# Performance work log

Measured on AMD Instinct MI355X. Metric: run time of the kernel, lower is better.

Reference implementation:

```python
import jax, jax.numpy as jnp
import numpy as np

N = 50000
E = 800000

def _glorot(k, shape):
    lim = float(np.sqrt(6.0 / (shape[0] + shape[1])))
    return jax.random.uniform(k, shape, jnp.float32, -lim, lim)

def setup_inputs() -> dict:
    key = jax.random.key(0)
    ks = jax.random.split(key, 12)
    x = jax.random.normal(ks[0], (N, 58), jnp.float32)
    edge_index = jax.random.randint(ks[1], (2, E), 0, N, jnp.int32)
    neg_edge_index = jax.random.randint(ks[2], (2, E), 0, N, jnp.int32)
    return dict(
        x=x, edge_index=edge_index, neg_edge_index=neg_edge_index,
        W1_0=_glorot(ks[3], (58, 300)), W1_1=_glorot(ks[4], (58, 300)), b1=jnp.zeros((300,), jnp.float32),
        W2_0=_glorot(ks[5], (300, 100)), W2_1=_glorot(ks[6], (300, 100)), b2=jnp.zeros((100,), jnp.float32),
        W3_0=_glorot(ks[7], (100, 1)), W3_1=_glorot(ks[8], (100, 1)), b3=jnp.zeros((1,), jnp.float32),
        lin1_W=_glorot(ks[9], (100, 58)), lin1_b=jnp.zeros((100,), jnp.float32),
        lin2_W=_glorot(ks[10], (100, 58)), lin2_b=jnp.zeros((100,), jnp.float32),
        c1=jnp.full((1,), 0.5, jnp.float32), c2=jnp.full((1,), 0.5, jnp.float32),
    )

def _cheb(x, src, dst, norm, W0, W1, b):
    tx1 = jax.ops.segment_sum(x[src] * norm[:, None], dst, num_segments=x.shape[0])
    return x @ W0 + tx1 @ W1 + b

def reference(x, edge_index, neg_edge_index,
              W1_0, W1_1, b1, W2_0, W2_1, b2, W3_0, W3_1, b3,
              lin1_W, lin1_b, lin2_W, lin2_b, c1, c2):
    src, dst = edge_index[0], edge_index[1]
    deg = jax.ops.segment_sum(jnp.ones((E,), x.dtype), src, num_segments=N)
    dis = jnp.where(deg > 0, 1.0 / jnp.sqrt(jnp.where(deg > 0, deg, 1.0)), 0.0)
    norm = -(dis[src] * dis[dst])  # [E]
    h = jax.nn.relu(_cheb(x, src, dst, norm, W1_0, W1_1, b1))      # [N,300]
    x1 = jax.nn.relu(_cheb(h, src, dst, norm, W2_0, W2_1, b2))     # [N,100]
    xm = x1 + jax.nn.relu(x @ lin1_W.T + lin1_b)
    z = x1 + jax.nn.relu(x @ lin2_W.T + lin2_b)
    pos_score = jnp.sum(z[edge_index[0]] * z[edge_index[1]], axis=1)
    pos_loss = -jnp.mean(jnp.log(jax.nn.sigmoid(pos_score) + 1e-15))
    neg_score = jnp.sum(z[neg_edge_index[0]] * z[neg_edge_index[1]], axis=1)
    neg_loss = -jnp.mean(jnp.log(1.0 - jax.nn.sigmoid(neg_score) + 1e-15))
    r_loss = pos_loss + neg_loss
    out = _cheb(xm, src, dst, norm, W3_0, W3_1, b3)                # [N,1]
    return (out, r_loss, c1, c2)
```

## Files before the change

### kernel.cpp

```cpp
#include <hip/hip_runtime.h>
#include <math.h>

#define NN 50000
#define NE 800000
#define SB 1024
#define CAP 64

using bf16x8 = __attribute__((ext_vector_type(8))) short;
using f32x4  = __attribute__((ext_vector_type(4))) float;
using f32x2  = __attribute__((ext_vector_type(2))) float;
using i32x8  = __attribute__((ext_vector_type(8))) int;

__device__ __forceinline__ float b2f(short s) {
    union { unsigned u; float f; } v;
    v.u = ((unsigned)(unsigned short)s) << 16;
    return v.f;
}
__device__ __forceinline__ unsigned short f2b(float f) {
    union { float f; unsigned u; } v;
    v.f = f;
    unsigned r = v.u + 0x7fffu + ((v.u >> 16) & 1u);
    return (unsigned short)(r >> 16);
}
__device__ __forceinline__ unsigned char f2e4m3(float f) {
    return (unsigned char)(__builtin_amdgcn_cvt_pk_fp8_f32(f, f, 0, false) & 0xff);
}

__global__ void k_degs(const int* __restrict__ ei, int* __restrict__ degs) {
    int e = blockIdx.x * 256 + threadIdx.x;
    if (e < NE) atomicAdd(&degs[ei[e]], 1);
}

__global__ __launch_bounds__(256) void k_prep(const float* __restrict__ x,
                                              unsigned short* __restrict__ xcat,
                                              unsigned char* __restrict__ xf8,
                                              const int* __restrict__ degs,
                                              float* __restrict__ dis,
                                              const float* __restrict__ W1_0,
                                              const float* __restrict__ W1_1,
                                              const float* __restrict__ W2_0,
                                              const float* __restrict__ W2_1,
                                              const float* __restrict__ L1,
                                              const float* __restrict__ L2,
                                              unsigned short* __restrict__ Wt1f,
                                              unsigned short* __restrict__ Wt2f,
                                              unsigned short* __restrict__ Wtlf) {
    int b = blockIdx.x;
    if (b < 12500) {
        int t = b * 256 + threadIdx.x;
        int n = t >> 6, k = t & 63;
        float v = (k < 58) ? x[(size_t)n * 58 + k] : 0.0f;
        xcat[(size_t)n * 128 + k] = f2b(v);
        xf8[(size_t)n * 64 + k] = f2e4m3(v);
        return;
    }
    if (b < 12696) {
        int i = (b - 12500) * 256 + threadIdx.x;
        if (i < NN) {
            float d = (float)degs[i];
            dis[i] = d > 0.0f ? 1.0f / sqrtf(d) : 0.0f;
        }
        return;
    }
    int t = (b - 12696) * 256 + threadIdx.x;
    if (t < 40960) {
        int f = t >> 9, lane = (t >> 3) & 63, j = t & 7;
        int nt = f >> 2, s = f & 3;
        int ml = lane & 15, quad = lane >> 4;
        int k = s * 32 + quad * 8 + j;
        int col = nt * 16 + ml;
        float v = 0.0f;
        if (col < 300) {
            if (k < 58) v = W1_0[k * 300 + col];
            else if (k >= 64 && k < 122) v = W1_1[(k - 64) * 300 + col];
        }
        Wt1f[t] = f2b(v);
    } else if (t < 107520) {
        int u = t - 40960;
        int f = u >> 9, lane = (u >> 3) & 63, j = u & 7;
        int nt = f / 10, s = f - nt * 10;
        int ml = lane & 15, quad = lane >> 4;
        int k = s * 32 + quad * 8 + j;
        int col = nt * 16 + ml;
        float v = 0.0f;
        if (k < 300) {
            if (col < 100) v = W2_0[k * 100 + col];
            else if (col >= 104 && col < 204) v = W2_1[k * 100 + (col - 104)];
        }
        Wt2f[u] = f2b(v);
    } else if (t < 120832) {
        int u = t - 107520;
        int f = u >> 9, lane = (u >> 3) & 63, j = u & 7;
        int nt = f >> 1, s = f & 1;
        int ml = lane & 15, quad = lane >> 4;
        int k = s * 32 + quad * 8 + j;
        int col = nt * 16 + ml;
        float v = 0.0f;
        if (k < 58) {
            if (col < 100) v = L1[col * 58 + k];
            else if (col >= 104 && col < 204) v = L2[(col - 104) * 58 + k];
        }
        Wtlf[u] = f2b(v);
    }
}

__global__ void k_fillbkt(const int* __restrict__ ei, const float* __restrict__ dis,
                          int* __restrict__ cnt, unsigned* __restrict__ bkt) {
    int e = blockIdx.x * 256 + threadIdx.x;
    if (e < NE) {
        int s = ei[e], d = ei[NE + e];
        int slot = atomicAdd(&cnt[d], 1);
        if (slot < CAP) {
            float nm = -(dis[s] * dis[d]);
            bkt[(d << 6) + slot] = ((unsigned)f2b(nm) << 16) | (unsigned)s;
        }
    }
}

__global__ __launch_bounds__(256) void k_gather58(const int* __restrict__ cnt,
                                                  const unsigned* __restrict__ bkt,
                                                  const unsigned char* __restrict__ xf8,
                                                  unsigned short* __restrict__ xcat) {
    int t = blockIdx.x * 256 + threadIdx.x;
    int n = t >> 3, l = t & 7;
    if (n >= NN) return;
    int c = cnt[n]; if (c > CAP) c = CAP;
    int base = n << 6;
    float acc[8] = {0, 0, 0, 0, 0, 0, 0, 0};
    for (int i = 0; i < c; i++) {
        unsigned pv = bkt[base + i];
        float cc = b2f((short)(pv >> 16));
        uint2 u = *(const uint2*)(xf8 + (size_t)(pv & 0xFFFFu) * 64 + l * 8);
        f32x2 p0 = __builtin_amdgcn_cvt_pk_f32_fp8(u.x, false);
        f32x2 p1 = __builtin_amdgcn_cvt_pk_f32_fp8(u.x, true);
        f32x2 p2 = __builtin_amdgcn_cvt_pk_f32_fp8(u.y, false);
        f32x2 p3 = __builtin_amdgcn_cvt_pk_f32_fp8(u.y, true);
        acc[0] += cc * p0.x; acc[1] += cc * p0.y;
        acc[2] += cc * p1.x; acc[3] += cc * p1.y;
        acc[4] += cc * p2.x; acc[5] += cc * p2.y;
        acc[6] += cc * p3.x; acc[7] += cc * p3.y;
    }
    bf16x8 o;
#pragma unroll
    for (int j = 0; j < 8; j++) o[j] = (short)f2b(acc[j]);
    *(bf16x8*)(xcat + (size_t)n * 128 + 64 + l * 8) = o;
}

__global__ __launch_bounds__(256) void k_mm12(const unsigned short* __restrict__ xcat,
                                              const unsigned short* __restrict__ Wt1f,
                                              const float* __restrict__ b1,
                                              const unsigned short* __restrict__ Wt2f,
                                              float* __restrict__ hp,
                                              unsigned char* __restrict__ hwf8) {
    __shared__ __attribute__((aligned(16))) unsigned short hs[64 * 328];
    __shared__ __attribute__((aligned(16))) unsigned short bst[2][5120];
    int tid = threadIdx.x;
    int wave = tid >> 6, lane = tid & 63, ml = lane & 15, quad = lane >> 4;
    int row0 = blockIdx.x * 64;
    int rw = row0 + wave * 16;

    int ar = rw + ml; if (ar >= NN) ar = NN - 1;
    const bf16x8* Ap = (const bf16x8*)(xcat + (size_t)ar * 128 + quad * 8);
    bf16x8 a0 = Ap[0], a1 = Ap[4], a2 = Ap[8], a3 = Ap[12];

    ((bf16x8*)bst[0])[tid] = ((const bf16x8*)Wt1f)[tid];
    __syncthreads();

    for (int nt = 0; nt < 20; nt++) {
        if (nt + 1 < 20)
            ((bf16x8*)bst[(nt + 1) & 1])[tid] =
                ((const bf16x8*)(Wt1f + (size_t)(nt + 1) * 2048))[tid];
        const bf16x8* Bp = (const bf16x8*)bst[nt & 1];
        f32x4 acc = {0.f, 0.f, 0.f, 0.f};
        acc = __builtin_amdgcn_mfma_f32_16x16x32_bf16(a0, Bp[0 * 64 + lane], acc, 0, 0, 0);
        acc = __builtin_amdgcn_mfma_f32_16x16x32_bf16(a1, Bp[1 * 64 + lane], acc, 0, 0, 0);
        acc = __builtin_amdgcn_mfma_f32_16x16x32_bf16(a2, Bp[2 * 64 + lane], acc, 0, 0, 0);
        acc = __builtin_amdgcn_mfma_f32_16x16x32_bf16(a3, Bp[3 * 64 + lane], acc, 0, 0, 0);
        int col = nt * 16 + ml;
        float bias = (col < 300) ? b1[col] : 0.0f;
#pragma unroll
        for (int r = 0; r < 4; r++) {
            float v = acc[r] + bias;
            v = v > 0.0f ? v : 0.0f;
            if (col >= 300) v = 0.0f;
            hs[(wave * 16 + quad * 4 + r) * 328 + col] = f2b(v);
        }
        __syncthreads();
    }

    for (int i = tid; i < 640; i += 256)
        ((bf16x8*)bst[0])[i] = ((const bf16x8*)Wt2f)[i];
    bf16x8 A2[10];
#pragma unroll
    for (int s = 0; s < 10; s++)
        A2[s] = *(const bf16x8*)(hs + (wave * 16 + ml) * 328 + s * 32 + quad * 8);
    __syncthreads();

    for (int nt = 0; nt < 13; nt++) {
        if (nt + 1 < 13)
            for (int i = tid; i < 640; i += 256)
                ((bf16x8*)bst[(nt + 1) & 1])[i] =
                    ((const bf16x8*)(Wt2f + (size_t)(nt + 1) * 5120))[i];
        const bf16x8* Bp = (const bf16x8*)bst[nt & 1];
        f32x4 acc = {0.f, 0.f, 0.f, 0.f};
#pragma unroll
        for (int s = 0; s < 10; s++)
            acc = __builtin_amdgcn_mfma_f32_16x16x32_bf16(A2[s], Bp[s * 64 + lane], acc, 0, 0, 0);
        int j = nt * 16 + ml;
#pragma unroll
        for (int r = 0; r < 4; r++) {
            int row = rw + quad * 4 + r;
            if (row < NN) {
                if (j < 104) hp[(size_t)row * 104 + j] = acc[r];
                else hwf8[(size_t)row * 128 + (j - 104)] = f2e4m3(acc[r]);
            }
        }
        __syncthreads();
    }
}

__global__ __launch_bounds__(256) void k_gather100(const int* __restrict__ cnt,
                                                   const unsigned* __restrict__ bkt,
                                                   const unsigned char* __restrict__ hwf8,
                                                   float* __restrict__ tx2) {
    int t = blockIdx.x * 256 + threadIdx.x;
    int n = t >> 4, l = t & 15;
    if (n >= NN || l >= 13) return;
    int c = cnt[n]; if (c > CAP) c = CAP;
    int base = n << 6;
    float acc[8] = {0, 0, 0, 0, 0, 0, 0, 0};
    for (int i = 0; i < c; i++) {
        unsigned pv = bkt[base + i];
        float cc = b2f((short)(pv >> 16));
        uint2 u = *(const uint2*)(hwf8 + (size_t)(pv & 0xFFFFu) * 128 + l * 8);
        f32x2 p0 = __builtin_amdgcn_cvt_pk_f32_fp8(u.x, false);
        f32x2 p1 = __builtin_amdgcn_cvt_pk_f32_fp8(u.x, true);
        f32x2 p2 = __builtin_amdgcn_cvt_pk_f32_fp8(u.y, false);
        f32x2 p3 = __builtin_amdgcn_cvt_pk_f32_fp8(u.y, true);
        acc[0] += cc * p0.x; acc[1] += cc * p0.y;
        acc[2] += cc * p1.x; acc[3] += cc * p1.y;
        acc[4] += cc * p2.x; acc[5] += cc * p2.y;
        acc[6] += cc * p3.x; acc[7] += cc * p3.y;
    }
    f32x4 o0 = {acc[0], acc[1], acc[2], acc[3]};
    f32x4 o1 = {acc[4], acc[5], acc[6], acc[7]};
    *(f32x4*)(tx2 + (size_t)n * 104 + l * 8) = o0;
    *(f32x4*)(tx2 + (size_t)n * 104 + l * 8 + 4) = o1;
}

__global__ __launch_bounds__(256) void k_mmlin(const unsigned short* __restrict__ xcat,
                                               const unsigned short* __restrict__ Wtlf,
                                               const float* __restrict__ hp,
                                               const float* __restrict__ tx2,
                                               const float* __restrict__ b2,
                                               const float* __restrict__ l1b,
                                               const float* __restrict__ l2b,
                                               float* __restrict__ xm,
                                               unsigned char* __restrict__ zf8) {
    int wave = threadIdx.x >> 6, lane = threadIdx.x & 63;
    int row0 = blockIdx.x * 64 + wave * 16;
    if (row0 >= NN) return;
    int ml = lane & 15, quad = lane >> 4;
    const bf16x8* Ap = (const bf16x8*)(xcat + (size_t)(row0 + ml) * 128 + quad * 8);
    bf16x8 a0 = Ap[0], a1 = Ap[4];
    for (int nt = 0; nt < 13; nt++) {
        bf16x8 b0 = *(const bf16x8*)(Wtlf + (size_t)((nt * 2 + 0) * 64 + lane) * 8);
        bf16x8 b1f = *(const bf16x8*)(Wtlf + (size_t)((nt * 2 + 1) * 64 + lane) * 8);
        f32x4 acc = {0.f, 0.f, 0.f, 0.f};
        acc = __builtin_amdgcn_mfma_f32_16x16x32_bf16(a0, b0, acc, 0, 0, 0);
        acc = __builtin_amdgcn_mfma_f32_16x16x32_bf16(a1, b1f, acc, 0, 0, 0);
        int j = nt * 16 + ml;
        int jj = (j < 104) ? j : j - 104;
        float bb = 0.0f, lb = 0.0f;
        if (jj < 100) {
            bb = b2[jj];
            lb = (j < 104) ? l1b[jj] : l2b[jj];
        }
#pragma unroll
        for (int r = 0; r < 4; r++) {
            int row = row0 + quad * 4 + r;
            float x1v = hp[(size_t)row * 104 + jj] + tx2[(size_t)row * 104 + jj] + bb;
            x1v = x1v > 0.0f ? x1v : 0.0f;
            float lv = acc[r] + lb;
            lv = lv > 0.0f ? lv : 0.0f;
            float o = x1v + lv;
            if (j < 104) xm[(size_t)row * 104 + j] = o;
            else zf8[(size_t)row * 128 + (j - 104)] = f2e4m3(o);
        }
    }
}

__global__ __launch_bounds__(256) void k_score_l3(const unsigned char* __restrict__ zf8,
                                                  const int* __restrict__ ei,
                                                  const int* __restrict__ nei,
                                                  double* __restrict__ red,
                                                  const float* __restrict__ xm,
                                                  const float* __restrict__ W30,
                                                  const float* __restrict__ W31,
                                                  const float* __restrict__ b3,
                                                  float* __restrict__ out,
                                                  float* __restrict__ s) {
    int tid = threadIdx.x;
    int lane = tid & 63;
    int wid = (blockIdx.x * 256 + tid) >> 6;
    int nw = SB * 4;
    int ml = lane & 15, quad = lane >> 4;
    int dr = ml - quad * 4;
    bool diag = (dr >= 0 && dr < 4);
    float facc = 0.0f;
    const int G = (2 * NE) / 16;
    for (int g = wid; g < G; g += nw) {
        int base = g * 16;
        int a, b;
        if (base < NE) {
            a = ei[base + ml];
            b = ei[NE + base + ml];
        } else {
            a = nei[base - NE + ml];
            b = nei[base + ml];
        }
        i32x8 av = *(const i32x8*)(zf8 + (size_t)a * 128 + quad * 32);
        i32x8 bv = *(const i32x8*)(zf8 + (size_t)b * 128 + quad * 32);
        f32x4 d = {0.f, 0.f, 0.f, 0.f};
        d = __builtin_amdgcn_mfma_scale_f32_16x16x128_f8f6f4(
                av, bv, d, 0, 0, 0, 0x7f7f7f7f, 0, 0x7f7f7f7f);
        if (diag) {
            float p = d[dr];
            float sg = 1.0f / (1.0f + expf(-p));
            float term = (base < NE) ? logf(sg + 1e-15f) : logf(1.0f - sg + 1e-15f);
            facc += term;
        }
    }
    int l32 = tid & 31;
    int gslot = (blockIdx.x * 256 + tid) >> 5;
    for (int n = gslot; n < NN; n += SB * 8) {
        const float* row = xm + (size_t)n * 104;
        float d0 = 0.0f, d1 = 0.0f;
        for (int k = l32; k < 100; k += 32) {
            float v = row[k];
            d0 += v * W30[k];
            d1 += v * W31[k];
        }
        for (int off = 16; off; off >>= 1) {
            d0 += __shfl_down(d0, off, 32);
            d1 += __shfl_down(d1, off, 32);
        }
        if (l32 == 0) {
            out[n] = d0 + b3[0];
            s[n] = d1;
        }
    }
    __shared__ double sred[256];
    sred[tid] = (double)facc;
    __syncthreads();
    for (int st = 128; st; st >>= 1) {
        if (tid < st) sred[tid] += sred[tid + st];
        __syncthreads();
    }
    if (tid == 0) red[blockIdx.x] = sred[0];
}

__global__ __launch_bounds__(256) void k_final_g1(const double* __restrict__ red,
                                                  const float* __restrict__ c1,
                                                  const float* __restrict__ c2,
                                                  const int* __restrict__ cnt,
                                                  const unsigned* __restrict__ bkt,
                                                  const float* __restrict__ s,
                                                  float* __restrict__ out) {
    if (blockIdx.x == 0) {
        double a = 0.0;
        for (int i = threadIdx.x; i < SB; i += 256) a += red[i];
        __shared__ double sred[256];
        sred[threadIdx.x] = a;
        __syncthreads();
        for (int st = 128; st; st >>= 1) {
            if (threadIdx.x < st) sred[threadIdx.x] += sred[threadIdx.x + st];
            __syncthreads();
        }
        if (threadIdx.x == 0) {
            out[NN] = (float)(-sred[0] / (double)NE);
            out[NN + 1] = c1[0];
            out[NN + 2] = c2[0];
        }
        return;
    }
    int n = (blockIdx.x - 1) * 256 + threadIdx.x;
    if (n >= NN) return;
    int c = cnt[n]; if (c > CAP) c = CAP;
    int base = n << 6;
    float acc = 0.0f;
    for (int i = 0; i < c; i++) {
        unsigned pv = bkt[base + i];
        acc += b2f((short)(pv >> 16)) * s[pv & 0xFFFFu];
    }
    out[n] += acc;
}

extern "C" void kernel_launch(void* const* d_in, const int* in_sizes, int n_in,
                              void* d_out, int out_size, void* d_ws, size_t ws_size,
                              hipStream_t stream) {
    const float* x    = (const float*)d_in[0];
    const int*   ei   = (const int*)d_in[1];
    const int*   nei  = (const int*)d_in[2];
    const float* W1_0 = (const float*)d_in[3];
    const float* W1_1 = (const float*)d_in[4];
    const float* b1   = (const float*)d_in[5];
    const float* W2_0 = (const float*)d_in[6];
    const float* W2_1 = (const float*)d_in[7];
    const float* b2   = (const float*)d_in[8];
    const float* W3_0 = (const float*)d_in[9];
    const float* W3_1 = (const float*)d_in[10];
    const float* b3   = (const float*)d_in[11];
    const float* l1W  = (const float*)d_in[12];
    const float* l1b  = (const float*)d_in[13];
    const float* l2W  = (const float*)d_in[14];
    const float* l2b  = (const float*)d_in[15];
    const float* c1   = (const float*)d_in[16];
    const float* c2   = (const float*)d_in[17];
    float* out = (float*)d_out;
    float* w = (float*)d_ws;

    unsigned*       bkt    = (unsigned*)w;
    int*            degs   = (int*)(w + 3200000);
    int*            cnt    = (int*)(w + 3250000);
    float*          dis    = w + 3300000;
    float*          sbuf   = w + 3350000;
    double*         red    = (double*)(w + 3400000);
    unsigned short* xcat   = (unsigned short*)(w + 3402048);
    unsigned short* Wt1f   = (unsigned short*)(w + 6602048);
    unsigned short* Wt2f   = (unsigned short*)(w + 6622528);
    unsigned short* Wtlf   = (unsigned short*)(w + 6655808);
    float*          hp     = w + 6662464;
    unsigned char*  hwf8   = (unsigned char*)(w + 11862464);
    float*          xm     = w + 13462464;
    unsigned char*  zf8    = (unsigned char*)(w + 18662464);
    unsigned char*  xf8    = (unsigned char*)(w + 20262464);
    float*          tx2    = w + 21062464;

    hipMemsetAsync(degs, 0, 100000 * sizeof(int), stream);

    k_degs<<<(NE + 255) / 256, 256, 0, stream>>>(ei, degs);
    k_prep<<<13168, 256, 0, stream>>>(x, xcat, xf8, degs, dis,
                                      W1_0, W1_1, W2_0, W2_1, l1W, l2W,
                                      Wt1f, Wt2f, Wtlf);
    k_fillbkt<<<(NE + 255) / 256, 256, 0, stream>>>(ei, dis, cnt, bkt);

    k_gather58<<<(NN * 8 + 255) / 256, 256, 0, stream>>>(cnt, bkt, xf8, xcat);
    k_mm12<<<(NN + 63) / 64, 256, 0, stream>>>(xcat, Wt1f, b1, Wt2f, hp, hwf8);

    k_gather100<<<NN * 16 / 256, 256, 0, stream>>>(cnt, bkt, hwf8, tx2);
    k_mmlin<<<(NN + 63) / 64, 256, 0, stream>>>(xcat, Wtlf, hp, tx2, b2, l1b, l2b, xm, zf8);

    k_score_l3<<<SB, 256, 0, stream>>>(zf8, ei, nei, red, xm, W3_0, W3_1, b3, out, sbuf);
    k_final_g1<<<1 + (NN + 255) / 256, 256, 0, stream>>>(red, c1, c2, cnt, bkt, sbuf, out);
}
```

Baseline: 382.1 us.

## Factor edge norm into node scaling, fuse gather100 into mmlin, split score/loss

The symmetric normalization is factored into per-node scaling: source features are pre-scaled by dis[src] and the aggregate is scaled by -dis[dst]. Buckets therefore store only 16-bit source indices, and degree counting and bucket fill merge into one kernel. The layer-2 gather moves into the linear/epilogue kernel through shared memory, and the W3 projection is done there too, so the tx2 and xm round trips disappear. Edge scoring now writes raw scores to a buffer and a separate loss kernel reduces them. This adds an extra pass over 1.6M floats and extra launches, and fp8 quantization now applies to scaled values.

```diff
diff --git a/kernel.cpp b/kernel.cpp
--- a/kernel.cpp
+++ b/kernel.cpp
@@ -3,7 +3,8 @@
 
 #define NN 50000
 #define NE 800000
-#define SB 1024
+#define SB2 2048
+#define LB 1024
 #define CAP 64
 
 using bf16x8 = __attribute__((ext_vector_type(8))) short;
@@ -25,10 +26,26 @@
 __device__ __forceinline__ unsigned char f2e4m3(float f) {
     return (unsigned char)(__builtin_amdgcn_cvt_pk_fp8_f32(f, f, 0, false) & 0xff);
 }
-
-__global__ void k_degs(const int* __restrict__ ei, int* __restrict__ degs) {
+__device__ __forceinline__ void acc8(float* acc, uint2 u) {
+    f32x2 p0 = __builtin_amdgcn_cvt_pk_f32_fp8(u.x, false);
+    f32x2 p1 = __builtin_amdgcn_cvt_pk_f32_fp8(u.x, true);
+    f32x2 p2 = __builtin_amdgcn_cvt_pk_f32_fp8(u.y, false);
+    f32x2 p3 = __builtin_amdgcn_cvt_pk_f32_fp8(u.y, true);
+    acc[0] += p0.x; acc[1] += p0.y;
+    acc[2] += p1.x; acc[3] += p1.y;
+    acc[4] += p2.x; acc[5] += p2.y;
+    acc[6] += p3.x; acc[7] += p3.y;
+}
+
+__global__ void k_build(const int* __restrict__ ei, int* __restrict__ degs,
+                        int* __restrict__ cnt, unsigned short* __restrict__ bkt16) {
     int e = blockIdx.x * 256 + threadIdx.x;
-    if (e < NE) atomicAdd(&degs[ei[e]], 1);
+    if (e < NE) {
+        int s = ei[e], d = ei[NE + e];
+        atomicAdd(&degs[s], 1);
+        int slot = atomicAdd(&cnt[d], 1);
+        if (slot < CAP) bkt16[(d << 6) + slot] = (unsigned short)s;
+    }
 }
 
 __global__ __launch_bounds__(256) void k_prep(const float* __restrict__ x,
@@ -51,14 +68,16 @@
         int n = t >> 6, k = t & 63;
         float v = (k < 58) ? x[(size_t)n * 58 + k] : 0.0f;
         xcat[(size_t)n * 128 + k] = f2b(v);
-        xf8[(size_t)n * 64 + k] = f2e4m3(v);
+        int dg = degs[n];
+        float dv = dg > 0 ? 1.0f / sqrtf((float)dg) : 0.0f;
+        xf8[(size_t)n * 64 + k] = f2e4m3(dv * v);
         return;
     }
     if (b < 12696) {
         int i = (b - 12500) * 256 + threadIdx.x;
         if (i < NN) {
-            float d = (float)degs[i];
-            dis[i] = d > 0.0f ? 1.0f / sqrtf(d) : 0.0f;
+            int dg = degs[i];
+            dis[i] = dg > 0 ? 1.0f / sqrtf((float)dg) : 0.0f;
         }
         return;
     }
@@ -104,45 +123,26 @@
     }
 }
 
-__global__ void k_fillbkt(const int* __restrict__ ei, const float* __restrict__ dis,
-                          int* __restrict__ cnt, unsigned* __restrict__ bkt) {
-    int e = blockIdx.x * 256 + threadIdx.x;
-    if (e < NE) {
-        int s = ei[e], d = ei[NE + e];
-        int slot = atomicAdd(&cnt[d], 1);
-        if (slot < CAP) {
-            float nm = -(dis[s] * dis[d]);
-            bkt[(d << 6) + slot] = ((unsigned)f2b(nm) << 16) | (unsigned)s;
-        }
-    }
-}
-
 __global__ __launch_bounds__(256) void k_gather58(const int* __restrict__ cnt,
-                                                  const unsigned* __restrict__ bkt,
+                                                  const unsigned short* __restrict__ bkt16,
+                                                  const float* __restrict__ dis,
                                                   const unsigned char* __restrict__ xf8,
                                                   unsigned short* __restrict__ xcat) {
     int t = blockIdx.x * 256 + threadIdx.x;
     int n = t >> 3, l = t & 7;
     if (n >= NN) return;
     int c = cnt[n]; if (c > CAP) c = CAP;
-    int base = n << 6;
+    float dn = dis[n];
+    const unsigned short* bp = bkt16 + (n << 6);
     float acc[8] = {0, 0, 0, 0, 0, 0, 0, 0};
     for (int i = 0; i < c; i++) {
-        unsigned pv = bkt[base + i];
-        float cc = b2f((short)(pv >> 16));
-        uint2 u = *(const uint2*)(xf8 + (size_t)(pv & 0xFFFFu) * 64 + l * 8);
-        f32x2 p0 = __builtin_amdgcn_cvt_pk_f32_fp8(u.x, false);
-        f32x2 p1 = __builtin_amdgcn_cvt_pk_f32_fp8(u.x, true);
-        f32x2 p2 = __builtin_amdgcn_cvt_pk_f32_fp8(u.y, false);
-        f32x2 p3 = __builtin_amdgcn_cvt_pk_f32_fp8(u.y, true);
-        acc[0] += cc * p0.x; acc[1] += cc * p0.y;
-        acc[2] += cc * p1.x; acc[3] += cc * p1.y;
-        acc[4] += cc * p2.x; acc[5] += cc * p2.y;
-        acc[6] += cc * p3.x; acc[7] += cc * p3.y;
+        unsigned src = bp[i];
+        uint2 u = *(const uint2*)(xf8 + (size_t)src * 64 + l * 8);
+        acc8(acc, u);
     }
     bf16x8 o;
 #pragma unroll
-    for (int j = 0; j < 8; j++) o[j] = (short)f2b(acc[j]);
+    for (int j = 0; j < 8; j++) o[j] = (short)f2b(-dn * acc[j]);
     *(bf16x8*)(xcat + (size_t)n * 128 + 64 + l * 8) = o;
 }
 
@@ -150,6 +150,7 @@
                                               const unsigned short* __restrict__ Wt1f,
                                               const float* __restrict__ b1,
                                               const unsigned short* __restrict__ Wt2f,
+                                              const float* __restrict__ dis,
                                               float* __restrict__ hp,
                                               unsigned char* __restrict__ hwf8) {
     __shared__ __attribute__((aligned(16))) unsigned short hs[64 * 328];
@@ -162,6 +163,12 @@
     int ar = rw + ml; if (ar >= NN) ar = NN - 1;
     const bf16x8* Ap = (const bf16x8*)(xcat + (size_t)ar * 128 + quad * 8);
     bf16x8 a0 = Ap[0], a1 = Ap[4], a2 = Ap[8], a3 = Ap[12];
+    float dv[4];
+#pragma unroll
+    for (int r = 0; r < 4; r++) {
+        int row = rw + quad * 4 + r;
+        dv[r] = dis[row < NN ? row : NN - 1];
+    }
 
     ((bf16x8*)bst[0])[tid] = ((const bf16x8*)Wt1f)[tid];
     __syncthreads();
@@ -212,63 +219,69 @@
             int row = rw + quad * 4 + r;
             if (row < NN) {
                 if (j < 104) hp[(size_t)row * 104 + j] = acc[r];
-                else hwf8[(size_t)row * 128 + (j - 104)] = f2e4m3(acc[r]);
+                else hwf8[(size_t)row * 128 + (j - 104)] = f2e4m3(dv[r] * acc[r]);
             }
         }
         __syncthreads();
     }
 }
 
-__global__ __launch_bounds__(256) void k_gather100(const int* __restrict__ cnt,
-                                                   const unsigned* __restrict__ bkt,
-                                                   const unsigned char* __restrict__ hwf8,
-                                                   float* __restrict__ tx2) {
-    int t = blockIdx.x * 256 + threadIdx.x;
-    int n = t >> 4, l = t & 15;
-    if (n >= NN || l >= 13) return;
-    int c = cnt[n]; if (c > CAP) c = CAP;
-    int base = n << 6;
-    float acc[8] = {0, 0, 0, 0, 0, 0, 0, 0};
-    for (int i = 0; i < c; i++) {
-        unsigned pv = bkt[base + i];
-        float cc = b2f((short)(pv >> 16));
-        uint2 u = *(const uint2*)(hwf8 + (size_t)(pv & 0xFFFFu) * 128 + l * 8);
-        f32x2 p0 = __builtin_amdgcn_cvt_pk_f32_fp8(u.x, false);
-        f32x2 p1 = __builtin_amdgcn_cvt_pk_f32_fp8(u.x, true);
-        f32x2 p2 = __builtin_amdgcn_cvt_pk_f32_fp8(u.y, false);
-        f32x2 p3 = __builtin_amdgcn_cvt_pk_f32_fp8(u.y, true);
-        acc[0] += cc * p0.x; acc[1] += cc * p0.y;
-        acc[2] += cc * p1.x; acc[3] += cc * p1.y;
-        acc[4] += cc * p2.x; acc[5] += cc * p2.y;
-        acc[6] += cc * p3.x; acc[7] += cc * p3.y;
-    }
-    f32x4 o0 = {acc[0], acc[1], acc[2], acc[3]};
-    f32x4 o1 = {acc[4], acc[5], acc[6], acc[7]};
-    *(f32x4*)(tx2 + (size_t)n * 104 + l * 8) = o0;
-    *(f32x4*)(tx2 + (size_t)n * 104 + l * 8 + 4) = o1;
-}
-
-__global__ __launch_bounds__(256) void k_mmlin(const unsigned short* __restrict__ xcat,
-                                               const unsigned short* __restrict__ Wtlf,
-                                               const float* __restrict__ hp,
-                                               const float* __restrict__ tx2,
-                                               const float* __restrict__ b2,
-                                               const float* __restrict__ l1b,
-                                               const float* __restrict__ l2b,
-                                               float* __restrict__ xm,
-                                               unsigned char* __restrict__ zf8) {
-    int wave = threadIdx.x >> 6, lane = threadIdx.x & 63;
-    int row0 = blockIdx.x * 64 + wave * 16;
-    if (row0 >= NN) return;
-    int ml = lane & 15, quad = lane >> 4;
-    const bf16x8* Ap = (const bf16x8*)(xcat + (size_t)(row0 + ml) * 128 + quad * 8);
+__global__ __launch_bounds__(256) void k_mmlin2(const unsigned short* __restrict__ xcat,
+                                                const unsigned short* __restrict__ Wtlf,
+                                                const float* __restrict__ hp,
+                                                const unsigned char* __restrict__ hwf8,
+                                                const int* __restrict__ cnt,
+                                                const unsigned short* __restrict__ bkt16,
+                                                const float* __restrict__ dis,
+                                                const float* __restrict__ b2,
+                                                const float* __restrict__ l1b,
+                                                const float* __restrict__ l2b,
+                                                const float* __restrict__ W30,
+                                                const float* __restrict__ W31,
+                                                const float* __restrict__ b3,
+                                                float* __restrict__ out,
+                                                float* __restrict__ qbuf,
+                                                unsigned char* __restrict__ zf8) {
+    __shared__ float tx2s[64 * 104];
+    int tid = threadIdx.x;
+    int wave = tid >> 6, lane = tid & 63, ml = lane & 15, quad = lane >> 4;
+    int row0 = blockIdx.x * 64;
+    int rw = row0 + wave * 16;
+
+    {
+        int l = tid & 15, nd0 = tid >> 4;
+        for (int sub = 0; sub < 4; sub++) {
+            int nd = sub * 16 + nd0;
+            int node = row0 + nd;
+            if (node < NN && l < 13) {
+                int c = cnt[node]; if (c > CAP) c = CAP;
+                float dn = dis[node];
+                const unsigned short* bp = bkt16 + (node << 6);
+                float acc[8] = {0, 0, 0, 0, 0, 0, 0, 0};
+                for (int i = 0; i < c; i++) {
+                    unsigned src = bp[i];
+                    uint2 u = *(const uint2*)(hwf8 + (size_t)src * 128 + l * 8);
+                    acc8(acc, u);
+                }
+#pragma unroll
+                for (int j = 0; j < 8; j++) tx2s[nd * 104 + l * 8 + j] = -dn * acc[j];
+            }
+        }
+    }
+    __syncthreads();
+
+    int ar = rw + ml; if (ar >= NN) ar = NN - 1;
+    const bf16x8* Ap = (const bf16x8*)(xcat + (size_t)ar * 128 + quad * 8);
     bf16x8 a0 = Ap[0], a1 = Ap[4];
+    float p0[4] = {0, 0, 0, 0}, p1[4] = {0, 0, 0, 0};
+    float b3v = b3[0];
+
     for (int nt = 0; nt < 13; nt++) {
-        bf16x8 b0 = *(const bf16x8*)(Wtlf + (size_t)((nt * 2 + 0) * 64 + lane) * 8);
-        bf16x8 b1f = *(const bf16x8*)(Wtlf + (size_t)((nt * 2 + 1) * 64 + lane) * 8);
+        bf16x8 bw0 = *(const bf16x8*)(Wtlf + (size_t)((nt * 2 + 0) * 64 + lane) * 8);
+        bf16x8 bw1 = *(const bf16x8*)(Wtlf + (size_t)((nt * 2 + 1) * 64 + lane) * 8);
         f32x4 acc = {0.f, 0.f, 0.f, 0.f};
-        acc = __builtin_amdgcn_mfma_f32_16x16x32_bf16(a0, b0, acc, 0, 0, 0);
-        acc = __builtin_amdgcn_mfma_f32_16x16x32_bf16(a1, b1f, acc, 0, 0, 0);
+        acc = __builtin_amdgcn_mfma_f32_16x16x32_bf16(a0, bw0, acc, 0, 0, 0);
+        acc = __builtin_amdgcn_mfma_f32_16x16x32_bf16(a1, bw1, acc, 0, 0, 0);
         int j = nt * 16 + ml;
         int jj = (j < 104) ? j : j - 104;
         float bb = 0.0f, lb = 0.0f;
@@ -276,38 +289,59 @@
             bb = b2[jj];
             lb = (j < 104) ? l1b[jj] : l2b[jj];
         }
+        float w0 = (j < 100) ? W30[j] : 0.0f;
+        float w1 = (j < 100) ? W31[j] : 0.0f;
 #pragma unroll
         for (int r = 0; r < 4; r++) {
-            int row = row0 + quad * 4 + r;
-            float x1v = hp[(size_t)row * 104 + jj] + tx2[(size_t)row * 104 + jj] + bb;
+            int row = rw + quad * 4 + r;
+            int rcl = row < NN ? row : NN - 1;
+            float x1v = hp[(size_t)rcl * 104 + jj] + tx2s[(wave * 16 + quad * 4 + r) * 104 + jj] + bb;
             x1v = x1v > 0.0f ? x1v : 0.0f;
             float lv = acc[r] + lb;
             lv = lv > 0.0f ? lv : 0.0f;
             float o = x1v + lv;
-            if (j < 104) xm[(size_t)row * 104 + j] = o;
-            else zf8[(size_t)row * 128 + (j - 104)] = f2e4m3(o);
-        }
-    }
-}
-
-__global__ __launch_bounds__(256) void k_score_l3(const unsigned char* __restrict__ zf8,
-                                                  const int* __restrict__ ei,
-                                                  const int* __restrict__ nei,
-                                                  double* __restrict__ red,
-                                                  const float* __restrict__ xm,
-                                                  const float* __restrict__ W30,
-                                                  const float* __restrict__ W31,
-                                                  const float* __restrict__ b3,
-                                                  float* __restrict__ out,
-                                                  float* __restrict__ s) {
-    int tid = threadIdx.x;
-    int lane = tid & 63;
-    int wid = (blockIdx.x * 256 + tid) >> 6;
-    int nw = SB * 4;
+            if (j < 104) {
+                p0[r] += o * w0;
+                p1[r] += o * w1;
+            } else if (row < NN) {
+                zf8[(size_t)row * 128 + (j - 104)] = f2e4m3(o);
+            }
+        }
+    }
+#pragma unroll
+    for (int m = 1; m < 16; m <<= 1) {
+#pragma unroll
+        for (int r = 0; r < 4; r++) {
+            p0[r] += __shfl_xor(p0[r], m, 64);
+            p1[r] += __shfl_xor(p1[r], m, 64);
+        }
+    }
+    if (ml == 0) {
+#pragma unroll
+        for (int r = 0; r < 4; r++) {
+            int row = rw + quad * 4 + r;
+            if (row < NN) {
+                out[row] = p0[r] + b3v;
+                qbuf[row] = dis[row] * p1[r];
+            }
+        }
+    }
+    for (int idx = tid; idx < 64 * 6; idx += 256) {
+        int rr = row0 + idx / 6;
+        if (rr < NN) *(unsigned*)(zf8 + (size_t)rr * 128 + 104 + (idx % 6) * 4) = 0u;
+    }
+}
+
+__global__ __launch_bounds__(256) void k_score(const unsigned char* __restrict__ zf8,
+                                               const int* __restrict__ ei,
+                                               const int* __restrict__ nei,
+                                               float* __restrict__ pbuf) {
+    int lane = threadIdx.x & 63;
+    int wid = (blockIdx.x * 256 + threadIdx.x) >> 6;
+    int nw = SB2 * 4;
     int ml = lane & 15, quad = lane >> 4;
     int dr = ml - quad * 4;
     bool diag = (dr >= 0 && dr < 4);
-    float facc = 0.0f;
     const int G = (2 * NE) / 16;
     for (int g = wid; g < G; g += nw) {
         int base = g * 16;
@@ -324,52 +358,40 @@
         f32x4 d = {0.f, 0.f, 0.f, 0.f};
         d = __builtin_amdgcn_mfma_scale_f32_16x16x128_f8f6f4(
                 av, bv, d, 0, 0, 0, 0x7f7f7f7f, 0, 0x7f7f7f7f);
-        if (diag) {
-            float p = d[dr];
-            float sg = 1.0f / (1.0f + expf(-p));
-            float term = (base < NE) ? logf(sg + 1e-15f) : logf(1.0f - sg + 1e-15f);
-            facc += term;
-        }
-    }
-    int l32 = tid & 31;
-    int gslot = (blockIdx.x * 256 + tid) >> 5;
-    for (int n = gslot; n < NN; n += SB * 8) {
-        const float* row = xm + (size_t)n * 104;
-        float d0 = 0.0f, d1 = 0.0f;
-        for (int k = l32; k < 100; k += 32) {
-            float v = row[k];
-            d0 += v * W30[k];
-            d1 += v * W31[k];
-        }
-        for (int off = 16; off; off >>= 1) {
-            d0 += __shfl_down(d0, off, 32);
-            d1 += __shfl_down(d1, off, 32);
-        }
-        if (l32 == 0) {
-            out[n] = d0 + b3[0];
-            s[n] = d1;
-        }
+        if (diag) pbuf[base + ml] = d[dr];
+    }
+}
+
+__global__ __launch_bounds__(256) void k_loss(const float* __restrict__ pbuf,
+                                              double* __restrict__ red) {
+    double acc = 0.0;
+    for (int i = blockIdx.x * 256 + threadIdx.x; i < 2 * NE; i += LB * 256) {
+        float p = pbuf[i];
+        float sg = 1.0f / (1.0f + expf(-p));
+        float term = (i < NE) ? logf(sg + 1e-15f) : logf(1.0f - sg + 1e-15f);
+        acc += (double)term;
     }
     __shared__ double sred[256];
-    sred[tid] = (double)facc;
+    sred[threadIdx.x] = acc;
     __syncthreads();
-    for (int st = 128; st; st >>= 1) {
-        if (tid < st) sred[tid] += sred[tid + st];
+    for (int s = 128; s; s >>= 1) {
+        if (threadIdx.x < s) sred[threadIdx.x] += sred[threadIdx.x + s];
         __syncthreads();
     }
-    if (tid == 0) red[blockIdx.x] = sred[0];
+    if (threadIdx.x == 0) red[blockIdx.x] = sred[0];
 }
 
 __global__ __launch_bounds__(256) void k_final_g1(const double* __restrict__ red,
                                                   const float* __restrict__ c1,
                                                   const float* __restrict__ c2,
                                                   const int* __restrict__ cnt,
-                                                  const unsigned* __restrict__ bkt,
-                                                  const float* __restrict__ s,
+                                                  const unsigned short* __restrict__ bkt16,
+                                                  const float* __restrict__ dis,
+                                                  const float* __restrict__ qbuf,
                                                   float* __restrict__ out) {
     if (blockIdx.x == 0) {
         double a = 0.0;
-        for (int i = threadIdx.x; i < SB; i += 256) a += red[i];
+        for (int i = threadIdx.x; i < LB; i += 256) a += red[i];
         __shared__ double sred[256];
         sred[threadIdx.x] = a;
         __syncthreads();
@@ -387,13 +409,10 @@
     int n = (blockIdx.x - 1) * 256 + threadIdx.x;
     if (n >= NN) return;
     int c = cnt[n]; if (c > CAP) c = CAP;
-    int base = n << 6;
+    const unsigned short* bp = bkt16 + (n << 6);
     float acc = 0.0f;
-    for (int i = 0; i < c; i++) {
-        unsigned pv = bkt[base + i];
-        acc += b2f((short)(pv >> 16)) * s[pv & 0xFFFFu];
-    }
-    out[n] += acc;
+    for (int i = 0; i < c; i++) acc += qbuf[bp[i]];
+    out[n] += -dis[n] * acc;
 }
 
 extern "C" void kernel_launch(void* const* d_in, const int* in_sizes, int n_in,
@@ -420,37 +439,37 @@
     float* out = (float*)d_out;
     float* w = (float*)d_ws;
 
-    unsigned*       bkt    = (unsigned*)w;
-    int*            degs   = (int*)(w + 3200000);
-    int*            cnt    = (int*)(w + 3250000);
-    float*          dis    = w + 3300000;
-    float*          sbuf   = w + 3350000;
-    double*         red    = (double*)(w + 3400000);
+    unsigned short* bkt16  = (unsigned short*)w;
+    int*            degs   = (int*)(w + 1600000);
+    int*            cnt    = (int*)(w + 1650000);
+    float*          dis    = w + 1700000;
+    float*          qbuf   = w + 1750000;
+    double*         red    = (double*)(w + 1800000);
+    float*          pbuf   = w + 1802048;
     unsigned short* xcat   = (unsigned short*)(w + 3402048);
     unsigned short* Wt1f   = (unsigned short*)(w + 6602048);
     unsigned short* Wt2f   = (unsigned short*)(w + 6622528);
     unsigned short* Wtlf   = (unsigned short*)(w + 6655808);
     float*          hp     = w + 6662464;
     unsigned char*  hwf8   = (unsigned char*)(w + 11862464);
-    float*          xm     = w + 13462464;
-    unsigned char*  zf8    = (unsigned char*)(w + 18662464);
-    unsigned char*  xf8    = (unsigned char*)(w + 20262464);
-    float*          tx2    = w + 21062464;
+    unsigned char*  zf8    = (unsigned char*)(w + 13462464);
+    unsigned char*  xf8    = (unsigned char*)(w + 15062464);
 
     hipMemsetAsync(degs, 0, 100000 * sizeof(int), stream);
 
-    k_degs<<<(NE + 255) / 256, 256, 0, stream>>>(ei, degs);
+    k_build<<<(NE + 255) / 256, 256, 0, stream>>>(ei, degs, cnt, bkt16);
     k_prep<<<13168, 256, 0, stream>>>(x, xcat, xf8, degs, dis,
                                       W1_0, W1_1, W2_0, W2_1, l1W, l2W,
                                       Wt1f, Wt2f, Wtlf);
-    k_fillbkt<<<(NE + 255) / 256, 256, 0, stream>>>(ei, dis, cnt, bkt);
-
-    k_gather58<<<(NN * 8 + 255) / 256, 256, 0, stream>>>(cnt, bkt, xf8, xcat);
-    k_mm12<<<(NN + 63) / 64, 256, 0, stream>>>(xcat, Wt1f, b1, Wt2f, hp, hwf8);
-
-    k_gather100<<<NN * 16 / 256, 256, 0, stream>>>(cnt, bkt, hwf8, tx2);
-    k_mmlin<<<(NN + 63) / 64, 256, 0, stream>>>(xcat, Wtlf, hp, tx2, b2, l1b, l2b, xm, zf8);
-
-    k_score_l3<<<SB, 256, 0, stream>>>(zf8, ei, nei, red, xm, W3_0, W3_1, b3, out, sbuf);
-    k_final_g1<<<1 + (NN + 255) / 256, 256, 0, stream>>>(red, c1, c2, cnt, bkt, sbuf, out);
-}
+
+    k_gather58<<<(NN * 8 + 255) / 256, 256, 0, stream>>>(cnt, bkt16, dis, xf8, xcat);
+    k_mm12<<<(NN + 63) / 64, 256, 0, stream>>>(xcat, Wt1f, b1, Wt2f, dis, hp, hwf8);
+
+    k_mmlin2<<<(NN + 63) / 64, 256, 0, stream>>>(xcat, Wtlf, hp, hwf8, cnt, bkt16, dis,
+                                                 b2, l1b, l2b, W3_0, W3_1, b3,
+                                                 out, qbuf, zf8);
+
+    k_score<<<SB2, 256, 0, stream>>>(zf8, ei, nei, pbuf);
+    k_loss<<<LB, 256, 0, stream>>>(pbuf, red);
+    k_final_g1<<<1 + (NN + 255) / 256, 256, 0, stream>>>(red, c1, c2, cnt, bkt16, dis, qbuf, out);
+}
```

Result: slower. 429.7 us (+12.5%).
